# Kernel optimization log

Measured on AMD Instinct MI355X. Metric: run time of the kernel, lower is better.

## Reference

```python
import jax, jax.numpy as jnp
import numpy as np

TOP_K = 4
TAU = 1.0  # training-mode temperature
EPS_NORM = 1e-12
EPS_G = 1e-10


def l2_normalize(x, axis=-1):
    sq = jnp.sum(x * x, axis=axis, keepdims=True)
    return x * jax.lax.rsqrt(jnp.maximum(sq, EPS_NORM))


def setup_inputs() -> dict:
    key = jax.random.key(0)
    k1, k2, k3, k4 = jax.random.split(key, 4)
    B, S, D = 256, 196, 1024
    P, L = 512, 8
    x_embed = jax.random.normal(k1, (B, S, D), dtype=jnp.float32)
    prompt = jax.random.normal(k2, (P, L, D), dtype=jnp.float32) * 0.02
    prompt_key = jax.random.normal(k3, (P, D), dtype=jnp.float32) * 0.02
    gumbel_u = jax.random.uniform(k4, (TOP_K, B, P), dtype=jnp.float32)
    return {"x_embed": x_embed, "prompt": prompt, "prompt_key": prompt_key,
            "gumbel_u": gumbel_u}


def reference(x_embed, prompt, prompt_key, gumbel_u):
    # query: mean over sequence dim (embedding_key='mean')  -> [B, D]
    query = jnp.mean(x_embed, axis=1)
    key_n = l2_normalize(prompt_key, axis=1)   # [P, D]
    q_n = l2_normalize(query, axis=1)          # [B, D]
    sim = jnp.matmul(q_n, key_n.T)             # [B, P]

    P = prompt.shape[0]
    cur = sim
    selected = []
    for i in range(TOP_K):
        # Gumbel(0,1) noise from uniform samples
        g = -jnp.log(-jnp.log(gumbel_u[i] + EPS_G) + EPS_G)
        soft = jax.nn.softmax((cur + g) / TAU, axis=-1)      # [B, P]
        hard = jax.nn.one_hot(jnp.argmax(soft, axis=-1), P, dtype=soft.dtype)
        w = soft + jax.lax.stop_gradient(hard - soft)        # straight-through
        # weighted combination over pool -> [B, L, D]
        sel = jnp.einsum('bp,pld->bld', w, prompt)
        selected.append(sel)
        # training-mode mask-out of selected entries
        cur = cur - w * 1000.0
    return jnp.concatenate(selected, axis=1)  # [B, TOP_K*L, D]
```

## Files before the change

kernel.cpp:

```cpp
#include <hip/hip_runtime.h>
#include <math.h>

#define B    256
#define S    196
#define D    1024
#define P    512
#define L    8
#define TOPK 4

#define SSPLIT 7
#define SCHUNK (S / SSPLIT)
#define KSPLIT 8

__global__ __launch_bounds__(256) void mean_partial_kernel(
    const float* __restrict__ x, float* __restrict__ part) {
  const int b = blockIdx.x;
  const int j = blockIdx.y;
  const int t = threadIdx.x;
  const float* xb = x + (size_t)b * S * D + (size_t)j * SCHUNK * D + t * 4;

  float4 acc = make_float4(0.f, 0.f, 0.f, 0.f);
#pragma unroll 4
  for (int s = 0; s < SCHUNK; ++s) {
    float4 v = *(const float4*)(xb + (size_t)s * D);
    acc.x += v.x; acc.y += v.y; acc.z += v.z; acc.w += v.w;
  }
  *(float4*)(part + ((size_t)b * SSPLIT + j) * D + t * 4) = acc;
}

__global__ __launch_bounds__(256) void norm_kernel(
    const float* __restrict__ part, const float* __restrict__ pk,
    float* __restrict__ qn, float* __restrict__ kn) {
  const int t = threadIdx.x;
  float4 acc;
  float* dst;

  if (blockIdx.x < B) {
    const int b = blockIdx.x;
    acc = make_float4(0.f, 0.f, 0.f, 0.f);
#pragma unroll
    for (int j = 0; j < SSPLIT; ++j) {
      float4 v = *(const float4*)(part + ((size_t)b * SSPLIT + j) * D + t * 4);
      acc.x += v.x; acc.y += v.y; acc.z += v.z; acc.w += v.w;
    }
    const float inv = 1.0f / (float)S;
    acc.x *= inv; acc.y *= inv; acc.z *= inv; acc.w *= inv;
    dst = qn + (size_t)b * D + t * 4;
  } else {
    const int p = blockIdx.x - B;
    acc = *(const float4*)(pk + (size_t)p * D + t * 4);
    dst = kn + (size_t)p * D + t * 4;
  }

  float ss = acc.x * acc.x + acc.y * acc.y + acc.z * acc.z + acc.w * acc.w;
  for (int off = 32; off > 0; off >>= 1) ss += __shfl_down(ss, off, 64);
  __shared__ float wsum[4];
  __shared__ float snorm;
  const int lane = t & 63, w = t >> 6;
  if (lane == 0) wsum[w] = ss;
  __syncthreads();
  if (t == 0) {
    float tot = wsum[0] + wsum[1] + wsum[2] + wsum[3];
    snorm = rsqrtf(fmaxf(tot, 1e-12f));
  }
  __syncthreads();
  const float r = snorm;
  *(float4*)dst = make_float4(acc.x * r, acc.y * r, acc.z * r, acc.w * r);
}

#define KK 16
__global__ __launch_bounds__(256) void sim_kernel(
    const float* __restrict__ qn, const float* __restrict__ kn,
    float* __restrict__ simp) {
  const int b0 = blockIdx.x * 64;
  const int p0 = blockIdx.y * 64;
  const int z  = blockIdx.z;
  const int k0 = z * (D / KSPLIT);
  const int t = threadIdx.x;
  const int tx = t & 15;
  const int ty = t >> 4;

  __shared__ float As[KK][68];
  __shared__ float Bs[KK][68];

  float acc[4][4];
#pragma unroll
  for (int i = 0; i < 4; ++i)
#pragma unroll
    for (int j = 0; j < 4; ++j) acc[i][j] = 0.f;

  const int rr = t >> 2;
  const int k4 = (t & 3) * 4;

  for (int kt = 0; kt < D / KSPLIT; kt += KK) {
    float4 a = *(const float4*)(qn + (size_t)(b0 + rr) * D + k0 + kt + k4);
    float4 bb = *(const float4*)(kn + (size_t)(p0 + rr) * D + k0 + kt + k4);
    As[k4 + 0][rr] = a.x; As[k4 + 1][rr] = a.y;
    As[k4 + 2][rr] = a.z; As[k4 + 3][rr] = a.w;
    Bs[k4 + 0][rr] = bb.x; Bs[k4 + 1][rr] = bb.y;
    Bs[k4 + 2][rr] = bb.z; Bs[k4 + 3][rr] = bb.w;
    __syncthreads();
#pragma unroll
    for (int kk = 0; kk < KK; ++kk) {
      float4 av = *(const float4*)&As[kk][ty * 4];
      float4 bv = *(const float4*)&Bs[kk][tx * 4];
      acc[0][0] += av.x * bv.x; acc[0][1] += av.x * bv.y;
      acc[0][2] += av.x * bv.z; acc[0][3] += av.x * bv.w;
      acc[1][0] += av.y * bv.x; acc[1][1] += av.y * bv.y;
      acc[1][2] += av.y * bv.z; acc[1][3] += av.y * bv.w;
      acc[2][0] += av.z * bv.x; acc[2][1] += av.z * bv.y;
      acc[2][2] += av.z * bv.z; acc[2][3] += av.z * bv.w;
      acc[3][0] += av.w * bv.x; acc[3][1] += av.w * bv.y;
      acc[3][2] += av.w * bv.z; acc[3][3] += av.w * bv.w;
    }
    __syncthreads();
  }
#pragma unroll
  for (int i = 0; i < 4; ++i)
#pragma unroll
    for (int j = 0; j < 4; ++j)
      simp[((size_t)z * B + b0 + ty * 4 + i) * P + p0 + tx * 4 + j] =
          acc[i][j];
}

__global__ __launch_bounds__(512) void select_kernel(
    const float* __restrict__ simp, const float* __restrict__ gu,
    int* __restrict__ sidx) {
  const int b = blockIdx.x;
  const int t = threadIdx.x;
  const int lane = t & 63, wv = t >> 6;

  float c = 0.f;
#pragma unroll
  for (int z = 0; z < KSPLIT; ++z)
    c += simp[((size_t)z * B + b) * P + t];

  float g[TOPK];
#pragma unroll
  for (int i = 0; i < TOPK; ++i) {
    float u = gu[((size_t)i * B + b) * P + t];
    g[i] = -logf(-logf(u + 1e-10f) + 1e-10f);
  }

  __shared__ float wval[8];
  __shared__ int   widx[8];
  __shared__ int   ssel[TOPK];

  for (int i = 0; i < TOPK; ++i) {
    float v = c + g[i];
    int idx = t;
    for (int off = 32; off > 0; off >>= 1) {
      float ov = __shfl_down(v, off, 64);
      int oi = __shfl_down(idx, off, 64);
      if (ov > v || (ov == v && oi < idx)) { v = ov; idx = oi; }
    }
    if (lane == 0) { wval[wv] = v; widx[wv] = idx; }
    __syncthreads();
    if (t == 0) {
      float bv = wval[0]; int bi = widx[0];
#pragma unroll
      for (int k = 1; k < 8; ++k)
        if (wval[k] > bv || (wval[k] == bv && widx[k] < bi)) {
          bv = wval[k]; bi = widx[k];
        }
      ssel[i] = bi;
    }
    __syncthreads();
    if (t == ssel[i]) c -= 1000.0f;
  }
  if (t < TOPK) sidx[b * TOPK + t] = ssel[t];
}

__global__ __launch_bounds__(256) void gather_kernel(
    const int* __restrict__ sidx, const float* __restrict__ prompt,
    float* __restrict__ out) {
  const int bi = blockIdx.x;
  const int h = blockIdx.y;
  const int t = threadIdx.x;
  const int p = sidx[bi];
  const float4* src =
      (const float4*)(prompt + (size_t)p * L * D) + h * 1024;
  float4* dst = (float4*)(out + (size_t)bi * (L * D)) + h * 1024;
#pragma unroll
  for (int c = 0; c < 4; ++c)
    dst[c * 256 + t] = src[c * 256 + t];
}

extern "C" void kernel_launch(void* const* d_in, const int* in_sizes, int n_in,
                              void* d_out, int out_size, void* d_ws,
                              size_t ws_size, hipStream_t stream) {
  const float* x_embed    = (const float*)d_in[0];
  const float* prompt     = (const float*)d_in[1];
  const float* prompt_key = (const float*)d_in[2];
  const float* gumbel_u   = (const float*)d_in[3];
  float* out = (float*)d_out;

  float* simp = (float*)d_ws;
  float* qn   = simp + (size_t)KSPLIT * B * P;
  float* kn   = qn + (size_t)B * D;
  float* part = kn + (size_t)P * D;
  int*   sidx = (int*)(part + (size_t)B * SSPLIT * D);

  mean_partial_kernel<<<dim3(B, SSPLIT), 256, 0, stream>>>(x_embed, part);
  norm_kernel<<<B + P, 256, 0, stream>>>(part, prompt_key, qn, kn);
  sim_kernel<<<dim3(B / 64, P / 64, KSPLIT), 256, 0, stream>>>(qn, kn, simp);
  select_kernel<<<B, 512, 0, stream>>>(simp, gumbel_u, sidx);
  gather_kernel<<<dim3(B * TOPK, 2), 256, 0, stream>>>(sidx, prompt, out);
}
```

Measured before the change: 332.0 us.

## Fuse mean and norm kernels, defer L2 normalization into select as scale factors

```diff
diff --git a/kernel.cpp b/kernel.cpp
--- a/kernel.cpp
+++ b/kernel.cpp
@@ -8,69 +8,72 @@
 #define L    8
 #define TOPK 4
 
-#define SSPLIT 7
-#define SCHUNK (S / SSPLIT)
 #define KSPLIT 8
-
-__global__ __launch_bounds__(256) void mean_partial_kernel(
-    const float* __restrict__ x, float* __restrict__ part) {
+#define RPG 49
+#define PKB 32
+#define PK_PER_BLOCK 16
+
+__global__ __launch_bounds__(1024) void query_norm_kernel(
+    const float* __restrict__ x, const float* __restrict__ pk,
+    float* __restrict__ qm, float* __restrict__ alpha,
+    float* __restrict__ beta) {
+  const int t = threadIdx.x;
+  const int lane = t & 63;
+  const int w = t >> 6;
+
+  if (blockIdx.x >= B) {
+    const int p = (blockIdx.x - B) * PK_PER_BLOCK + w;
+    const float* kp = pk + (size_t)p * D;
+    float ss = 0.f;
+#pragma unroll
+    for (int j = 0; j < 4; ++j) {
+      float4 v = *(const float4*)(kp + lane * 4 + j * 256);
+      ss += v.x * v.x + v.y * v.y + v.z * v.z + v.w * v.w;
+    }
+    for (int off = 32; off > 0; off >>= 1) ss += __shfl_down(ss, off, 64);
+    if (lane == 0) beta[p] = rsqrtf(fmaxf(ss, 1e-12f));
+    return;
+  }
+
   const int b = blockIdx.x;
-  const int j = blockIdx.y;
-  const int t = threadIdx.x;
-  const float* xb = x + (size_t)b * S * D + (size_t)j * SCHUNK * D + t * 4;
+  const int g = t >> 8;
+  const int c = t & 255;
+  const float* xb =
+      x + (size_t)b * S * D + (size_t)g * RPG * D + c * 4;
 
   float4 acc = make_float4(0.f, 0.f, 0.f, 0.f);
-#pragma unroll 4
-  for (int s = 0; s < SCHUNK; ++s) {
+#pragma unroll 7
+  for (int s = 0; s < RPG; ++s) {
     float4 v = *(const float4*)(xb + (size_t)s * D);
     acc.x += v.x; acc.y += v.y; acc.z += v.z; acc.w += v.w;
   }
-  *(float4*)(part + ((size_t)b * SSPLIT + j) * D + t * 4) = acc;
-}
-
-__global__ __launch_bounds__(256) void norm_kernel(
-    const float* __restrict__ part, const float* __restrict__ pk,
-    float* __restrict__ qn, float* __restrict__ kn) {
-  const int t = threadIdx.x;
-  float4 acc;
-  float* dst;
-
-  if (blockIdx.x < B) {
-    const int b = blockIdx.x;
-    acc = make_float4(0.f, 0.f, 0.f, 0.f);
-#pragma unroll
-    for (int j = 0; j < SSPLIT; ++j) {
-      float4 v = *(const float4*)(part + ((size_t)b * SSPLIT + j) * D + t * 4);
-      acc.x += v.x; acc.y += v.y; acc.z += v.z; acc.w += v.w;
-    }
+
+  __shared__ float4 red[3][256];
+  __shared__ float wsum[4];
+  if (g > 0) red[g - 1][c] = acc;
+  __syncthreads();
+
+  if (g == 0) {
+    float4 r0 = red[0][c], r1 = red[1][c], r2 = red[2][c];
+    acc.x += r0.x + r1.x + r2.x;
+    acc.y += r0.y + r1.y + r2.y;
+    acc.z += r0.z + r1.z + r2.z;
+    acc.w += r0.w + r1.w + r2.w;
     const float inv = 1.0f / (float)S;
     acc.x *= inv; acc.y *= inv; acc.z *= inv; acc.w *= inv;
-    dst = qn + (size_t)b * D + t * 4;
-  } else {
-    const int p = blockIdx.x - B;
-    acc = *(const float4*)(pk + (size_t)p * D + t * 4);
-    dst = kn + (size_t)p * D + t * 4;
-  }
-
-  float ss = acc.x * acc.x + acc.y * acc.y + acc.z * acc.z + acc.w * acc.w;
-  for (int off = 32; off > 0; off >>= 1) ss += __shfl_down(ss, off, 64);
-  __shared__ float wsum[4];
-  __shared__ float snorm;
-  const int lane = t & 63, w = t >> 6;
-  if (lane == 0) wsum[w] = ss;
+    *(float4*)(qm + (size_t)b * D + c * 4) = acc;
+    float ss = acc.x * acc.x + acc.y * acc.y + acc.z * acc.z + acc.w * acc.w;
+    for (int off = 32; off > 0; off >>= 1) ss += __shfl_down(ss, off, 64);
+    if (lane == 0) wsum[w] = ss;
+  }
   __syncthreads();
-  if (t == 0) {
-    float tot = wsum[0] + wsum[1] + wsum[2] + wsum[3];
-    snorm = rsqrtf(fmaxf(tot, 1e-12f));
-  }
-  __syncthreads();
-  const float r = snorm;
-  *(float4*)dst = make_float4(acc.x * r, acc.y * r, acc.z * r, acc.w * r);
+  if (t == 0)
+    alpha[b] = rsqrtf(fmaxf(wsum[0] + wsum[1] + wsum[2] + wsum[3], 1e-12f));
 }
 
 #define KK 16
 __global__ __launch_bounds__(256) void sim_kernel(
-    const float* __restrict__ qn, const float* __restrict__ kn,
+    const float* __restrict__ qm, const float* __restrict__ pk,
     float* __restrict__ simp) {
   const int b0 = blockIdx.x * 64;
   const int p0 = blockIdx.y * 64;
@@ -93,8 +96,8 @@
   const int k4 = (t & 3) * 4;
 
   for (int kt = 0; kt < D / KSPLIT; kt += KK) {
-    float4 a = *(const float4*)(qn + (size_t)(b0 + rr) * D + k0 + kt + k4);
-    float4 bb = *(const float4*)(kn + (size_t)(p0 + rr) * D + k0 + kt + k4);
+    float4 a = *(const float4*)(qm + (size_t)(b0 + rr) * D + k0 + kt + k4);
+    float4 bb = *(const float4*)(pk + (size_t)(p0 + rr) * D + k0 + kt + k4);
     As[k4 + 0][rr] = a.x; As[k4 + 1][rr] = a.y;
     As[k4 + 2][rr] = a.z; As[k4 + 3][rr] = a.w;
     Bs[k4 + 0][rr] = bb.x; Bs[k4 + 1][rr] = bb.y;
@@ -124,7 +127,8 @@
 }
 
 __global__ __launch_bounds__(512) void select_kernel(
-    const float* __restrict__ simp, const float* __restrict__ gu,
+    const float* __restrict__ simp, const float* __restrict__ alpha,
+    const float* __restrict__ beta, const float* __restrict__ gu,
     int* __restrict__ sidx) {
   const int b = blockIdx.x;
   const int t = threadIdx.x;
@@ -134,6 +138,7 @@
 #pragma unroll
   for (int z = 0; z < KSPLIT; ++z)
     c += simp[((size_t)z * B + b) * P + t];
+  c *= alpha[b] * beta[t];
 
   float g[TOPK];
 #pragma unroll
@@ -195,15 +200,16 @@
   const float* gumbel_u   = (const float*)d_in[3];
   float* out = (float*)d_out;
 
-  float* simp = (float*)d_ws;
-  float* qn   = simp + (size_t)KSPLIT * B * P;
-  float* kn   = qn + (size_t)B * D;
-  float* part = kn + (size_t)P * D;
-  int*   sidx = (int*)(part + (size_t)B * SSPLIT * D);
-
-  mean_partial_kernel<<<dim3(B, SSPLIT), 256, 0, stream>>>(x_embed, part);
-  norm_kernel<<<B + P, 256, 0, stream>>>(part, prompt_key, qn, kn);
-  sim_kernel<<<dim3(B / 64, P / 64, KSPLIT), 256, 0, stream>>>(qn, kn, simp);
-  select_kernel<<<B, 512, 0, stream>>>(simp, gumbel_u, sidx);
+  float* simp  = (float*)d_ws;
+  float* qm    = simp + (size_t)KSPLIT * B * P;
+  float* alpha = qm + (size_t)B * D;
+  float* beta  = alpha + B;
+  int*   sidx  = (int*)(beta + P);
+
+  query_norm_kernel<<<B + PKB, 1024, 0, stream>>>(x_embed, prompt_key, qm,
+                                                  alpha, beta);
+  sim_kernel<<<dim3(B / 64, P / 64, KSPLIT), 256, 0, stream>>>(qm, prompt_key,
+                                                               simp);
+  select_kernel<<<B, 512, 0, stream>>>(simp, alpha, beta, gumbel_u, sidx);
   gather_kernel<<<dim3(B * TOPK, 2), 256, 0, stream>>>(sidx, prompt, out);
 }
```

Result: no change. 327.2 us (-1.4%).

## Fold L2 normalization into post-matmul scaling and drop the norm kernel

Applied to the files above, without the earlier changes.

```diff
diff --git a/kernel.cpp b/kernel.cpp
--- a/kernel.cpp
+++ b/kernel.cpp
@@ -11,66 +11,49 @@
 #define SSPLIT 7
 #define SCHUNK (S / SSPLIT)
 #define KSPLIT 8
-
-__global__ __launch_bounds__(256) void mean_partial_kernel(
-    const float* __restrict__ x, float* __restrict__ part) {
-  const int b = blockIdx.x;
-  const int j = blockIdx.y;
-  const int t = threadIdx.x;
-  const float* xb = x + (size_t)b * S * D + (size_t)j * SCHUNK * D + t * 4;
-
-  float4 acc = make_float4(0.f, 0.f, 0.f, 0.f);
+#define KK 16
+#define NPART_BLK (B * SSPLIT)
+#define BETA_BLK 32
+
+__global__ __launch_bounds__(256) void k1_partial_beta_kernel(
+    const float* __restrict__ x, const float* __restrict__ pk,
+    float* __restrict__ part, float* __restrict__ beta) {
+  const int blk = blockIdx.x;
+  const int t = threadIdx.x;
+
+  if (blk < NPART_BLK) {
+    const int b = blk / SSPLIT;
+    const int j = blk % SSPLIT;
+    const float* xb =
+        x + (size_t)b * S * D + (size_t)j * SCHUNK * D + t * 4;
+    float4 acc = make_float4(0.f, 0.f, 0.f, 0.f);
 #pragma unroll 4
-  for (int s = 0; s < SCHUNK; ++s) {
-    float4 v = *(const float4*)(xb + (size_t)s * D);
-    acc.x += v.x; acc.y += v.y; acc.z += v.z; acc.w += v.w;
-  }
-  *(float4*)(part + ((size_t)b * SSPLIT + j) * D + t * 4) = acc;
-}
-
-__global__ __launch_bounds__(256) void norm_kernel(
+    for (int s = 0; s < SCHUNK; ++s) {
+      float4 v = *(const float4*)(xb + (size_t)s * D);
+      acc.x += v.x; acc.y += v.y; acc.z += v.z; acc.w += v.w;
+    }
+    *(float4*)(part + ((size_t)b * SSPLIT + j) * D + t * 4) = acc;
+  } else {
+    const int pb = blk - NPART_BLK;
+    const int lane = t & 63, w = t >> 6;
+#pragma unroll
+    for (int r = 0; r < 4; ++r) {
+      const int p = pb * 16 + w * 4 + r;
+      const float* kp = pk + (size_t)p * D;
+      float ss = 0.f;
+#pragma unroll
+      for (int j = 0; j < 4; ++j) {
+        float4 v = *(const float4*)(kp + lane * 4 + j * 256);
+        ss += v.x * v.x + v.y * v.y + v.z * v.z + v.w * v.w;
+      }
+      for (int off = 32; off > 0; off >>= 1) ss += __shfl_down(ss, off, 64);
+      if (lane == 0) beta[p] = rsqrtf(fmaxf(ss, 1e-12f));
+    }
+  }
+}
+
+__global__ __launch_bounds__(256) void sim_kernel(
     const float* __restrict__ part, const float* __restrict__ pk,
-    float* __restrict__ qn, float* __restrict__ kn) {
-  const int t = threadIdx.x;
-  float4 acc;
-  float* dst;
-
-  if (blockIdx.x < B) {
-    const int b = blockIdx.x;
-    acc = make_float4(0.f, 0.f, 0.f, 0.f);
-#pragma unroll
-    for (int j = 0; j < SSPLIT; ++j) {
-      float4 v = *(const float4*)(part + ((size_t)b * SSPLIT + j) * D + t * 4);
-      acc.x += v.x; acc.y += v.y; acc.z += v.z; acc.w += v.w;
-    }
-    const float inv = 1.0f / (float)S;
-    acc.x *= inv; acc.y *= inv; acc.z *= inv; acc.w *= inv;
-    dst = qn + (size_t)b * D + t * 4;
-  } else {
-    const int p = blockIdx.x - B;
-    acc = *(const float4*)(pk + (size_t)p * D + t * 4);
-    dst = kn + (size_t)p * D + t * 4;
-  }
-
-  float ss = acc.x * acc.x + acc.y * acc.y + acc.z * acc.z + acc.w * acc.w;
-  for (int off = 32; off > 0; off >>= 1) ss += __shfl_down(ss, off, 64);
-  __shared__ float wsum[4];
-  __shared__ float snorm;
-  const int lane = t & 63, w = t >> 6;
-  if (lane == 0) wsum[w] = ss;
-  __syncthreads();
-  if (t == 0) {
-    float tot = wsum[0] + wsum[1] + wsum[2] + wsum[3];
-    snorm = rsqrtf(fmaxf(tot, 1e-12f));
-  }
-  __syncthreads();
-  const float r = snorm;
-  *(float4*)dst = make_float4(acc.x * r, acc.y * r, acc.z * r, acc.w * r);
-}
-
-#define KK 16
-__global__ __launch_bounds__(256) void sim_kernel(
-    const float* __restrict__ qn, const float* __restrict__ kn,
     float* __restrict__ simp) {
   const int b0 = blockIdx.x * 64;
   const int p0 = blockIdx.y * 64;
@@ -93,8 +76,14 @@
   const int k4 = (t & 3) * 4;
 
   for (int kt = 0; kt < D / KSPLIT; kt += KK) {
-    float4 a = *(const float4*)(qn + (size_t)(b0 + rr) * D + k0 + kt + k4);
-    float4 bb = *(const float4*)(kn + (size_t)(p0 + rr) * D + k0 + kt + k4);
+    float4 a = make_float4(0.f, 0.f, 0.f, 0.f);
+    const float* pb = part + ((size_t)(b0 + rr) * SSPLIT) * D + k0 + kt + k4;
+#pragma unroll
+    for (int j = 0; j < SSPLIT; ++j) {
+      float4 v = *(const float4*)(pb + (size_t)j * D);
+      a.x += v.x; a.y += v.y; a.z += v.z; a.w += v.w;
+    }
+    float4 bb = *(const float4*)(pk + (size_t)(p0 + rr) * D + k0 + kt + k4);
     As[k4 + 0][rr] = a.x; As[k4 + 1][rr] = a.y;
     As[k4 + 2][rr] = a.z; As[k4 + 3][rr] = a.w;
     Bs[k4 + 0][rr] = bb.x; Bs[k4 + 1][rr] = bb.y;
@@ -124,16 +113,43 @@
 }
 
 __global__ __launch_bounds__(512) void select_kernel(
-    const float* __restrict__ simp, const float* __restrict__ gu,
+    const float* __restrict__ simp, const float* __restrict__ part,
+    const float* __restrict__ beta, const float* __restrict__ gu,
     int* __restrict__ sidx) {
   const int b = blockIdx.x;
   const int t = threadIdx.x;
   const int lane = t & 63, wv = t >> 6;
 
+  __shared__ float wval[8];
+  __shared__ int   widx[8];
+  __shared__ int   ssel[TOPK];
+  __shared__ float s_alpha;
+
+  float sq = 0.f;
+#pragma unroll
+  for (int d = t; d < D; d += 512) {
+    float s7 = 0.f;
+#pragma unroll
+    for (int j = 0; j < SSPLIT; ++j)
+      s7 += part[((size_t)b * SSPLIT + j) * D + d];
+    sq += s7 * s7;
+  }
+  for (int off = 32; off > 0; off >>= 1) sq += __shfl_down(sq, off, 64);
+  if (lane == 0) wval[wv] = sq;
+  __syncthreads();
+  if (t == 0) {
+    float tot = 0.f;
+#pragma unroll
+    for (int k = 0; k < 8; ++k) tot += wval[k];
+    s_alpha = rsqrtf(fmaxf(tot, 3.8416e-8f));
+  }
+  __syncthreads();
+
   float c = 0.f;
 #pragma unroll
   for (int z = 0; z < KSPLIT; ++z)
     c += simp[((size_t)z * B + b) * P + t];
+  c *= s_alpha * beta[t];
 
   float g[TOPK];
 #pragma unroll
@@ -141,10 +157,6 @@
     float u = gu[((size_t)i * B + b) * P + t];
     g[i] = -logf(-logf(u + 1e-10f) + 1e-10f);
   }
-
-  __shared__ float wval[8];
-  __shared__ int   widx[8];
-  __shared__ int   ssel[TOPK];
 
   for (int i = 0; i < TOPK; ++i) {
     float v = c + g[i];
@@ -196,14 +208,15 @@
   float* out = (float*)d_out;
 
   float* simp = (float*)d_ws;
-  float* qn   = simp + (size_t)KSPLIT * B * P;
-  float* kn   = qn + (size_t)B * D;
-  float* part = kn + (size_t)P * D;
-  int*   sidx = (int*)(part + (size_t)B * SSPLIT * D);
-
-  mean_partial_kernel<<<dim3(B, SSPLIT), 256, 0, stream>>>(x_embed, part);
-  norm_kernel<<<B + P, 256, 0, stream>>>(part, prompt_key, qn, kn);
-  sim_kernel<<<dim3(B / 64, P / 64, KSPLIT), 256, 0, stream>>>(qn, kn, simp);
-  select_kernel<<<B, 512, 0, stream>>>(simp, gumbel_u, sidx);
+  float* part = simp + (size_t)KSPLIT * B * P;
+  float* beta = part + (size_t)B * SSPLIT * D;
+  int*   sidx = (int*)(beta + P);
+
+  k1_partial_beta_kernel<<<NPART_BLK + BETA_BLK, 256, 0, stream>>>(
+      x_embed, prompt_key, part, beta);
+  sim_kernel<<<dim3(B / 64, P / 64, KSPLIT), 256, 0, stream>>>(part,
+                                                               prompt_key,
+                                                               simp);
+  select_kernel<<<B, 512, 0, stream>>>(simp, part, beta, gumbel_u, sidx);
   gather_kernel<<<dim3(B * TOPK, 2), 256, 0, stream>>>(sidx, prompt, out);
 }
```

After: 332.2 us. About the same (+0.1%).
